# Kernel optimization log

Measured on AMD Instinct MI355X. Metric: run time of the kernel, lower is better.

## Reference

```python
import jax, jax.numpy as jnp
import numpy as np

WORD_EMB = 300   # config.word_emb_size
SEN_EMB  = 256   # config.sen_emb_size (bidirectional -> 512)
DOC_EMB  = 256   # config.doc_emb_size (bidirectional -> 512)
SEN2, DOC2 = 2 * SEN_EMB, 2 * DOC_EMB
B, S, L, TL = 64, 10, 30, 15
VOCAB, NO_URLS = 50000, 64


def setup_inputs() -> dict:
    key = jax.random.key(0)
    ks = jax.random.split(key, 32)
    def nrm(k, shape, s=0.05):
        return jax.random.normal(k, shape, jnp.float32) * s
    inp = {}
    inp["input_ids"] = jax.random.randint(ks[0], (B, S, L), 0, VOCAB)
    inp["urls"]      = jax.random.randint(ks[1], (B, S), 0, NO_URLS)
    inp["titles"]    = jax.random.randint(ks[2], (B, TL), 0, VOCAB)
    inp["emb"] = nrm(ks[3], (VOCAB, WORD_EMB), 0.1)
    # sentence BiLSTM (PyTorch gate order i,f,g,o; b = b_ih + b_hh fused)
    inp["sen_wih_f"] = nrm(ks[4], (4 * SEN_EMB, WORD_EMB))
    inp["sen_whh_f"] = nrm(ks[5], (4 * SEN_EMB, SEN_EMB))
    inp["sen_b_f"]   = nrm(ks[6], (4 * SEN_EMB,))
    inp["sen_wih_b"] = nrm(ks[7], (4 * SEN_EMB, WORD_EMB))
    inp["sen_whh_b"] = nrm(ks[8], (4 * SEN_EMB, SEN_EMB))
    inp["sen_b_b"]   = nrm(ks[9], (4 * SEN_EMB,))
    # SourceBias per-url expert weights
    inp["trans"]   = nrm(ks[10], (NO_URLS, SEN2, SEN2))
    inp["sb_bias"] = nrm(ks[11], (NO_URLS, SEN2))
    # document BiLSTM
    inp["doc_wih_f"] = nrm(ks[12], (4 * DOC_EMB, SEN2))
    inp["doc_whh_f"] = nrm(ks[13], (4 * DOC_EMB, DOC_EMB))
    inp["doc_b_f"]   = nrm(ks[14], (4 * DOC_EMB,))
    inp["doc_wih_b"] = nrm(ks[15], (4 * DOC_EMB, SEN2))
    inp["doc_whh_b"] = nrm(ks[16], (4 * DOC_EMB, DOC_EMB))
    inp["doc_b_b"]   = nrm(ks[17], (4 * DOC_EMB,))
    # Bilinear attention: out = x W y + b, W:[DOC2, SEN2]
    inp["attn_W"] = nrm(ks[18], (DOC2, SEN2))
    inp["attn_b"] = nrm(ks[19], (1,))
    # bias MLP 512 -> 256 -> 5
    inp["bias_W1"] = nrm(ks[20], (DOC2 // 2, DOC2))
    inp["bias_b1"] = nrm(ks[21], (DOC2 // 2,))
    inp["bias_W2"] = nrm(ks[22], (5, DOC2 // 2))
    inp["bias_b2"] = nrm(ks[23], (5,))
    # truth MLP 512 -> 256 -> 1
    inp["truth_W1"] = nrm(ks[24], (DOC2 // 2, DOC2))
    inp["truth_b1"] = nrm(ks[25], (DOC2 // 2,))
    inp["truth_W2"] = nrm(ks[26], (1, DOC2 // 2))
    inp["truth_b2"] = nrm(ks[27], (1,))
    return inp


def _lstm_dir(x, w_ih, w_hh, b):
    # x: [N, T, E] -> (outputs [N, T, H], final hidden [N, H])
    N = x.shape[0]
    H = w_hh.shape[1]
    xw = jnp.einsum('nte,ge->ntg', x, w_ih) + b  # precompute input projection
    def step(carry, xw_t):
        h, c = carry
        gates = xw_t + h @ w_hh.T
        i, f, g, o = jnp.split(gates, 4, axis=-1)
        c = jax.nn.sigmoid(f) * c + jax.nn.sigmoid(i) * jnp.tanh(g)
        h = jax.nn.sigmoid(o) * jnp.tanh(c)
        return (h, c), h
    h0 = jnp.zeros((N, H), x.dtype)
    (hT, _), hs = jax.lax.scan(step, (h0, h0), jnp.swapaxes(xw, 0, 1))
    return jnp.swapaxes(hs, 0, 1), hT


def _bilstm(x, wf, hf, bf, wb, hb, bb):
    out_f, hT_f = _lstm_dir(x, wf, hf, bf)
    out_b, hT_b = _lstm_dir(x[:, ::-1], wb, hb, bb)
    out = jnp.concatenate([out_f, out_b[:, ::-1]], axis=-1)
    hT = jnp.concatenate([hT_f, hT_b], axis=-1)
    return out, hT


def reference(input_ids, urls, titles, emb,
              sen_wih_f, sen_whh_f, sen_b_f, sen_wih_b, sen_whh_b, sen_b_b,
              trans, sb_bias,
              doc_wih_f, doc_whh_f, doc_b_f, doc_wih_b, doc_whh_b, doc_b_b,
              attn_W, attn_b,
              bias_W1, bias_b1, bias_W2, bias_b2,
              truth_W1, truth_b1, truth_W2, truth_b2):
    # --- sentence encoder: [B,S,L] ids -> [B,S,SEN2] ---
    words = emb[input_ids.reshape(-1)].reshape(B * S, L, WORD_EMB)
    _, sen_h = _bilstm(words, sen_wih_f, sen_whh_f, sen_b_f,
                       sen_wih_b, sen_whh_b, sen_b_b)
    sentences = sen_h.reshape(B, S, SEN2)

    # --- SourceBias: per-token url-indexed weight matmul + bias + tanh ---
    u = urls.reshape(-1)                                  # [B*S]
    sen_flat = sentences.reshape(-1, SEN2)                # [B*S, SEN2]
    biased = jnp.tanh(
        jnp.einsum('td,tde->te', sen_flat, trans[u]) + sb_bias[u]
    ).reshape(B, S, SEN2)

    # --- document encoder over (source-biased) sentences ---
    documents, _ = _bilstm(biased, doc_wih_f, doc_whh_f, doc_b_f,
                           doc_wih_b, doc_whh_b, doc_b_b)  # [B,S,DOC2]

    # --- heading encoder: titles as a single sentence ---
    title_words = emb[titles.reshape(-1)].reshape(B, TL, WORD_EMB)
    _, headings = _bilstm(title_words, sen_wih_f, sen_whh_f, sen_b_f,
                          sen_wih_b, sen_whh_b, sen_b_b)   # [B, SEN2]

    # --- bilinear attention over sentences ---
    scores = jnp.einsum('bsd,de,be->bs', documents, attn_W, headings) + attn_b[0]
    w = jax.nn.softmax(scores, axis=1)                     # [B,S]
    doc_rep = jnp.einsum('bsd,bs->bd', documents, w)       # [B,DOC2]

    # --- heads ---
    h1 = jnp.tanh(doc_rep @ bias_W1.T + bias_b1)
    bias_out = jax.nn.softmax(jnp.tanh(h1 @ bias_W2.T + bias_b2), axis=1)
    t1 = jnp.tanh(doc_rep @ truth_W1.T + truth_b1)
    truth_out = jax.nn.sigmoid(jnp.tanh(t1 @ truth_W2.T + truth_b2))
    return bias_out, truth_out
```

## Files before the change

### kernel.cpp

```cpp
#include <hip/hip_runtime.h>
#include <cstddef>

typedef short bf16x8 __attribute__((ext_vector_type(8)));
typedef float f32x4 __attribute__((ext_vector_type(4)));

__device__ __forceinline__ float sigm(float x) {
    return __builtin_amdgcn_rcpf(1.f + __expf(-x));
}
__device__ __forceinline__ float ftanh(float x) {
    float e = __expf(2.f * x);
    return 1.f - 2.f * __builtin_amdgcn_rcpf(e + 1.f);
}

__device__ __forceinline__ unsigned short f2bf(float f) {
    union { float f; unsigned u; } v; v.f = f;
    return (unsigned short)((v.u + 0x7FFFu + ((v.u >> 16) & 1u)) >> 16);
}

#define N0 (20160 * 160)
#define N1 (2048 * 160)
#define N2 (2048 * 256)

__global__ __launch_bounds__(256) void prep_cast(
    const int* __restrict__ ids, const int* __restrict__ titles,
    const float* __restrict__ emb,
    const float* __restrict__ swf, const float* __restrict__ swb,
    const float* __restrict__ dwf, const float* __restrict__ dwb,
    unsigned* __restrict__ Abf, unsigned* __restrict__ Wsen,
    unsigned* __restrict__ Wdoc)
{
    int idx = blockIdx.x * 256 + threadIdx.x;
    if (idx < N0) {
        int row = idx / 160, kk = idx - row * 160;
        int id = (row < 19200) ? ids[row] : titles[row - 19200];
        float a = 0.f, b = 0.f;
        if (kk < 150) {
            const float* s = emb + (size_t)id * 300 + kk * 2;
            a = s[0]; b = s[1];
        }
        Abf[idx] = (unsigned)f2bf(a) | ((unsigned)f2bf(b) << 16);
    } else if (idx < N0 + N1) {
        int j = idx - N0;
        int row = j / 160, kk = j - row * 160;
        const float* base = (row < 1024) ? swf + (size_t)row * 300
                                         : swb + (size_t)(row - 1024) * 300;
        float a = 0.f, b = 0.f;
        if (kk < 150) { a = base[kk * 2]; b = base[kk * 2 + 1]; }
        Wsen[j] = (unsigned)f2bf(a) | ((unsigned)f2bf(b) << 16);
    } else if (idx < N0 + N1 + N2) {
        int j = idx - N0 - N1;
        int row = j >> 8, kk = j & 255;
        const float* base = (row < 1024) ? dwf + (size_t)row * 512
                                         : dwb + (size_t)(row - 1024) * 512;
        Wdoc[j] = (unsigned)f2bf(base[kk * 2]) | ((unsigned)f2bf(base[kk * 2 + 1]) << 16);
    }
}

__global__ __launch_bounds__(256) void prep_whh(
    const float* __restrict__ swf, const float* __restrict__ swb,
    const float* __restrict__ dwf, const float* __restrict__ dwb,
    unsigned* __restrict__ WS, unsigned* __restrict__ WD)
{
    int idx = blockIdx.x * 256 + threadIdx.x;
    const float* src; unsigned* dst;
    if (idx < 262144) {
        int j = idx; int dir = j >> 17; int rem = j & 131071;
        src = (dir ? swb : swf) + ((size_t)(rem >> 7) * 256 + (rem & 127) * 2);
        dst = WS + j;
    } else {
        int j = idx - 262144; int dir = j >> 17; int rem = j & 131071;
        src = (dir ? dwb : dwf) + ((size_t)(rem >> 7) * 256 + (rem & 127) * 2);
        dst = WD + j;
    }
    *dst = (unsigned)f2bf(src[0]) | ((unsigned)f2bf(src[1]) << 16);
}

__global__ __launch_bounds__(256) void proj_mfma(
    const unsigned short* __restrict__ Abf, int M, int Kp,
    const unsigned short* __restrict__ Wbf,
    const float* __restrict__ bf_, const float* __restrict__ bb_,
    float* __restrict__ out)
{
    __shared__ unsigned short As[128 * 40];
    __shared__ unsigned short Ws[128 * 40];
    const int tid  = threadIdx.x;
    const int lane = tid & 63;
    const int w    = tid >> 6;
    const int n    = lane & 15;
    const int quad = lane >> 4;
    const int bm   = blockIdx.x * 128;
    const int by   = blockIdx.y;
    const int half = by >> 3;
    const int ug32 = (by & 7) * 32;
    const unsigned short* Wb = Wbf + (size_t)half * 1024 * Kp;
    const float* biasp = half ? bb_ : bf_;

    f32x4 acc[2][8];
#pragma unroll
    for (int rt = 0; rt < 2; rt++)
#pragma unroll
        for (int ct = 0; ct < 8; ct++) acc[rt][ct] = (f32x4){0.f, 0.f, 0.f, 0.f};

    const int chunks = Kp >> 5;
    for (int kc = 0; kc < chunks; kc++) {
        const int k0 = kc * 32;
#pragma unroll
        for (int j = 0; j < 2; j++) {
            int idx = j * 256 + tid;
            int arow = idx >> 2, qq = idx & 3;
            int grow = bm + arow; if (grow >= M) grow = M - 1;
            *(uint4*)&As[arow * 40 + qq * 8] =
                *(const uint4*)(Abf + (size_t)grow * Kp + k0 + qq * 8);
            int cc = idx >> 2;
            int wrow = (cc >> 5) * 256 + ug32 + (cc & 31);
            *(uint4*)&Ws[cc * 40 + qq * 8] =
                *(const uint4*)(Wb + (size_t)wrow * Kp + k0 + qq * 8);
        }
        __syncthreads();
        bf16x8 Aq[2], Bq[8];
#pragma unroll
        for (int rt = 0; rt < 2; rt++)
            Aq[rt] = *(const bf16x8*)&As[((w * 2 + rt) * 16 + n) * 40 + quad * 8];
#pragma unroll
        for (int ct = 0; ct < 8; ct++)
            Bq[ct] = *(const bf16x8*)&Ws[(ct * 16 + n) * 40 + quad * 8];
#pragma unroll
        for (int rt = 0; rt < 2; rt++)
#pragma unroll
            for (int ct = 0; ct < 8; ct++)
                acc[rt][ct] = __builtin_amdgcn_mfma_f32_16x16x32_bf16(
                    Aq[rt], Bq[ct], acc[rt][ct], 0, 0, 0);
        __syncthreads();
    }

#pragma unroll
    for (int s = 0; s < 2; s++) {
        const int uL = s * 16 + n;
        float b0 = biasp[ug32 + uL];
        float b1 = biasp[256 + ug32 + uL];
        float b2 = biasp[512 + ug32 + uL];
        float b3 = biasp[768 + ug32 + uL];
#pragma unroll
        for (int rt = 0; rt < 2; rt++) {
#pragma unroll
            for (int r = 0; r < 4; r++) {
                int row = bm + (w * 2 + rt) * 16 + quad * 4 + r;
                if (row >= M) continue;
                float4 o;
                o.x = acc[rt][0 + s][r] + b0;
                o.y = acc[rt][2 + s][r] + b1;
                o.z = acc[rt][4 + s][r] + b2;
                o.w = acc[rt][6 + s][r] + b3;
                *(float4*)(out + (size_t)row * 2048 + half * 1024 + (ug32 + uL) * 4) = o;
            }
        }
    }
}

__device__ __forceinline__ void pair_sync(unsigned* cnt, unsigned target) {
    __syncthreads();
    if (threadIdx.x == 0) {
        __hip_atomic_fetch_add(cnt, 1u, __ATOMIC_RELAXED, __HIP_MEMORY_SCOPE_AGENT);
        while (__hip_atomic_load(cnt, __ATOMIC_RELAXED, __HIP_MEMORY_SCOPE_AGENT) < target)
            __builtin_amdgcn_s_sleep(1);
    }
    __syncthreads();
}

__device__ __forceinline__ const float* sen_xbase(
    const float* xw, const float* xw_head, int grow_e, int t)
{
    if (grow_e < 640)       return xw + ((size_t)grow_e * 30 + t) * 2048;
    else if (grow_e < 1280) return xw + ((size_t)(grow_e - 640) * 30 + 29 - t) * 2048 + 1024;
    else if (grow_e < 1344) return xw_head + ((size_t)(grow_e - 1280) * 15 + t) * 2048;
    else                    return xw_head + ((size_t)(grow_e - 1344) * 15 + 14 - t) * 2048 + 1024;
}

__global__ __launch_bounds__(512, 2) void lstm_sen2b(
    const float* __restrict__ xw, const float* __restrict__ xw_head,
    const unsigned short* __restrict__ WhhBf,
    unsigned short* hbA, unsigned short* hbB,
    float* __restrict__ sentences, float* __restrict__ headings,
    unsigned* bars)
{
    const int tid  = threadIdx.x;
    const int lane = tid & 63;
    const int w    = tid >> 6;
    const int n    = lane & 15;
    const int quad = lane >> 4;
    const int phys = blockIdx.x;
    const int g    = (phys & 7) + (phys >> 4) * 8;
    const int p    = (phys >> 3) & 1;
    const int r0   = g * 16;
    const bool bwd  = (r0 >= 640 && r0 < 1280) || (r0 >= 1344);
    const bool head = (r0 >= 1280);
    const int tEnd = head ? 15 : 30;
    unsigned* cnt = bars + g * 16;
    const unsigned short* Wd = WhhBf + (bwd ? (size_t)262144 : 0);

    __shared__ unsigned short Hs[2][16][264];
    __shared__ float G[16][516];

    bf16x8 Bf[4][8];
#pragma unroll
    for (int ct = 0; ct < 4; ct++) {
        const int c    = ct * 16 + n;
        const int unit = p * 128 + w * 16 + (c >> 2);
        const int wrow = (c & 3) * 256 + unit;
        const unsigned short* wr = Wd + (size_t)wrow * 256;
#pragma unroll
        for (int ks = 0; ks < 8; ks++)
            Bf[ct][ks] = *(const bf16x8*)(wr + ks * 32 + quad * 8);
    }

    for (int i = tid; i < 16 * 264; i += 512) ((unsigned short*)Hs[0])[i] = 0;

    const int rE  = tid & 15;
    const int iE  = tid >> 4;
    const int ug4 = p * 128 + iE * 4;
    const int grow_e = r0 + rE;
    float cr[4] = {0.f, 0.f, 0.f, 0.f};

    const float* xptr = sen_xbase(xw, xw_head, grow_e, 0) + (size_t)ug4 * 4;
    const long long xstep = bwd ? -2048 : 2048;
    float4 xv[4];
    { const float4* xp = (const float4*)xptr;
      xv[0] = xp[0]; xv[1] = xp[1]; xv[2] = xp[2]; xv[3] = xp[3]; }

    float* fdst;
    if (!head) fdst = sentences + (size_t)(bwd ? grow_e - 640 : grow_e) * 512
                      + (bwd ? 256 : 0) + ug4;
    else       fdst = headings + (size_t)(grow_e - (bwd ? 1344 : 1280)) * 512
                      + (bwd ? 256 : 0) + ug4;

    __syncthreads();

    for (int t = 0; t < tEnd; t++) {
        const int cur = t & 1;
        unsigned short* hq = (t & 1) ? hbA : hbB;

        {
            bf16x8 Af[8];
#pragma unroll
            for (int ks = 0; ks < 8; ks++)
                Af[ks] = *(const bf16x8*)&Hs[cur][n][ks * 32 + quad * 8];
            f32x4 acc[4];
#pragma unroll
            for (int ct = 0; ct < 4; ct++) acc[ct] = (f32x4){0.f, 0.f, 0.f, 0.f};
#pragma unroll
            for (int ks = 0; ks < 8; ks++)
#pragma unroll
                for (int ct = 0; ct < 4; ct++)
                    acc[ct] = __builtin_amdgcn_mfma_f32_16x16x32_bf16(
                        Af[ks], Bf[ct][ks], acc[ct], 0, 0, 0);
#pragma unroll
            for (int ct = 0; ct < 4; ct++)
#pragma unroll
                for (int r = 0; r < 4; r++)
                    G[quad * 4 + r][w * 64 + ct * 16 + n] = acc[ct][r];
        }
        __syncthreads();

        {
            const float4* Gp = (const float4*)&G[rE][iE * 16];
            unsigned long long hpack = 0ull;
            float hout[4];
#pragma unroll
            for (int q2 = 0; q2 < 4; q2++) {
                float4 gv = Gp[q2];
                float gi = gv.x + xv[q2].x;
                float gf = gv.y + xv[q2].y;
                float gg = gv.z + xv[q2].z;
                float go = gv.w + xv[q2].w;
                float cn = sigm(gf) * cr[q2] + sigm(gi) * ftanh(gg);
                float hn = sigm(go) * ftanh(cn);
                cr[q2] = cn; hout[q2] = hn;
                hpack |= ((unsigned long long)f2bf(hn)) << (16 * q2);
            }
            const int nxt = cur ^ 1;
            *(unsigned long long*)&Hs[nxt][rE][ug4] = hpack;
            __hip_atomic_store((unsigned long long*)(hq + (size_t)grow_e * 256 + ug4),
                               hpack, __ATOMIC_RELAXED, __HIP_MEMORY_SCOPE_AGENT);
            if (t == tEnd - 1) *(float4*)fdst = *(float4*)hout;
        }

        if (t + 1 < tEnd) {
            xptr += xstep;
            const float4* xp = (const float4*)xptr;
            xv[0] = xp[0]; xv[1] = xp[1]; xv[2] = xp[2]; xv[3] = xp[3];
            pair_sync(cnt, 2u * (unsigned)(t + 1));
            {
                const int nxt   = cur ^ 1;
                const int row   = tid >> 5;
                const int chunk = tid & 31;
                const int pp    = p ^ 1;
                unsigned long long v = __hip_atomic_load(
                    (const unsigned long long*)(hq + (size_t)(r0 + row) * 256
                                                + pp * 128 + chunk * 4),
                    __ATOMIC_RELAXED, __HIP_MEMORY_SCOPE_AGENT);
                *(unsigned long long*)&Hs[nxt][row][pp * 128 + chunk * 4] = v;
            }
            __syncthreads();
        }
    }
}

__global__ __launch_bounds__(512, 2) void lstm_doc2b(
    const float* __restrict__ xw,
    const unsigned short* __restrict__ WhhBf,
    unsigned short* hdA, unsigned short* hdB,
    float* __restrict__ documents,
    unsigned* bars)
{
    const int tid  = threadIdx.x;
    const int lane = tid & 63;
    const int w    = tid >> 6;
    const int n    = lane & 15;
    const int quad = lane >> 4;
    const int phys = blockIdx.x;
    const int g    = phys & 7;
    const int p    = (phys >> 3) & 1;
    const int r0   = g * 16;
    const bool bwd = (r0 >= 64);
    unsigned* cnt = bars + g * 16;
    const unsigned short* Wd = WhhBf + (bwd ? (size_t)262144 : 0);

    __shared__ unsigned short Hs[2][16][264];
    __shared__ float G[16][516];

    bf16x8 Bf[4][8];
#pragma unroll
    for (int ct = 0; ct < 4; ct++) {
        const int c    = ct * 16 + n;
        const int unit = p * 128 + w * 16 + (c >> 2);
        const int wrow = (c & 3) * 256 + unit;
        const unsigned short* wr = Wd + (size_t)wrow * 256;
#pragma unroll
        for (int ks = 0; ks < 8; ks++)
            Bf[ct][ks] = *(const bf16x8*)(wr + ks * 32 + quad * 8);
    }

    for (int i = tid; i < 16 * 264; i += 512) ((unsigned short*)Hs[0])[i] = 0;

    const int rE  = tid & 15;
    const int iE  = tid >> 4;
    const int ug4 = p * 128 + iE * 4;
    const int grow_e = r0 + rE;
    const int seq = bwd ? grow_e - 64 : grow_e;
    float cr[4] = {0.f, 0.f, 0.f, 0.f};

    const float* xptr = (!bwd ? xw + (size_t)seq * 10 * 2048
                              : xw + ((size_t)seq * 10 + 9) * 2048 + 1024)
                        + (size_t)ug4 * 4;
    const long long xstep = bwd ? -2048 : 2048;
    float4 xv[4];
    { const float4* xp = (const float4*)xptr;
      xv[0] = xp[0]; xv[1] = xp[1]; xv[2] = xp[2]; xv[3] = xp[3]; }

    float* dptr = documents + (size_t)(seq * 10 + (bwd ? 9 : 0)) * 512
                  + (bwd ? 256 : 0) + ug4;
    const long long dstep = bwd ? -512 : 512;

    __syncthreads();

    for (int t = 0; t < 10; t++) {
        const int cur = t & 1;
        unsigned short* hq = (t & 1) ? hdA : hdB;

        {
            bf16x8 Af[8];
#pragma unroll
            for (int ks = 0; ks < 8; ks++)
                Af[ks] = *(const bf16x8*)&Hs[cur][n][ks * 32 + quad * 8];
            f32x4 acc[4];
#pragma unroll
            for (int ct = 0; ct < 4; ct++) acc[ct] = (f32x4){0.f, 0.f, 0.f, 0.f};
#pragma unroll
            for (int ks = 0; ks < 8; ks++)
#pragma unroll
                for (int ct = 0; ct < 4; ct++)
                    acc[ct] = __builtin_amdgcn_mfma_f32_16x16x32_bf16(
                        Af[ks], Bf[ct][ks], acc[ct], 0, 0, 0);
#pragma unroll
            for (int ct = 0; ct < 4; ct++)
#pragma unroll
                for (int r = 0; r < 4; r++)
                    G[quad * 4 + r][w * 64 + ct * 16 + n] = acc[ct][r];
        }
        __syncthreads();

        {
            const float4* Gp = (const float4*)&G[rE][iE * 16];
            unsigned long long hpack = 0ull;
            float hout[4];
#pragma unroll
            for (int q2 = 0; q2 < 4; q2++) {
                float4 gv = Gp[q2];
                float gi = gv.x + xv[q2].x;
                float gf = gv.y + xv[q2].y;
                float gg = gv.z + xv[q2].z;
                float go = gv.w + xv[q2].w;
                float cn = sigm(gf) * cr[q2] + sigm(gi) * ftanh(gg);
                float hn = sigm(go) * ftanh(cn);
                cr[q2] = cn; hout[q2] = hn;
                hpack |= ((unsigned long long)f2bf(hn)) << (16 * q2);
            }
            const int nxt = cur ^ 1;
            *(unsigned long long*)&Hs[nxt][rE][ug4] = hpack;
            __hip_atomic_store((unsigned long long*)(hq + (size_t)grow_e * 256 + ug4),
                               hpack, __ATOMIC_RELAXED, __HIP_MEMORY_SCOPE_AGENT);
            *(float4*)dptr = *(float4*)hout;
        }

        if (t < 9) {
            xptr += xstep;  dptr += dstep;
            const float4* xp = (const float4*)xptr;
            xv[0] = xp[0]; xv[1] = xp[1]; xv[2] = xp[2]; xv[3] = xp[3];
            pair_sync(cnt, 2u * (unsigned)(t + 1));
            {
                const int nxt   = cur ^ 1;
                const int row   = tid >> 5;
                const int chunk = tid & 31;
                const int pp    = p ^ 1;
                unsigned long long v = __hip_atomic_load(
                    (const unsigned long long*)(hq + (size_t)(r0 + row) * 256
                                                + pp * 128 + chunk * 4),
                    __ATOMIC_RELAXED, __HIP_MEMORY_SCOPE_AGENT);
                *(unsigned long long*)&Hs[nxt][row][pp * 128 + chunk * 4] = v;
            }
            __syncthreads();
        }
    }
}

__global__ __launch_bounds__(256) void source_bias(
    const float* __restrict__ sentences, const int* __restrict__ urls,
    const float* __restrict__ trans, const float* __restrict__ sb_bias,
    unsigned* __restrict__ biasedBf)
{
    const int tkn = blockIdx.x;
    const int u = urls[tkn];
    const float2* Tm = (const float2*)(trans + (size_t)u * 512 * 512);
    __shared__ float sv[512];
    for (int i = threadIdx.x; i < 512; i += 256) sv[i] = sentences[(size_t)tkn * 512 + i];
    __syncthreads();
    const int e = threadIdx.x;
    float ax = 0.f, ay = 0.f;
#pragma unroll 4
    for (int d = 0; d < 512; d++) {
        float s = sv[d];
        float2 tv = Tm[(size_t)d * 256 + e];
        ax += s * tv.x; ay += s * tv.y;
    }
    const float2 bv = ((const float2*)(sb_bias + (size_t)u * 512))[e];
    float x = ftanh(ax + bv.x), y = ftanh(ay + bv.y);
    biasedBf[(size_t)tkn * 256 + e] = (unsigned)f2bf(x) | ((unsigned)f2bf(y) << 16);
}

__global__ __launch_bounds__(256) void attn_v(
    const float* __restrict__ W, const float* __restrict__ headings,
    float* __restrict__ v)
{
    const int b = blockIdx.x;
    __shared__ float hh[512];
    for (int i = threadIdx.x; i < 512; i += 256) hh[i] = headings[(size_t)b * 512 + i];
    __syncthreads();
    for (int d = threadIdx.x; d < 512; d += 256) {
        float a = 0.f;
        const float* wr = W + (size_t)d * 512;
        for (int e = 0; e < 512; e++) a += wr[e] * hh[e];
        v[(size_t)b * 512 + d] = a;
    }
}

__global__ __launch_bounds__(256) void attn_heads(
    const float* __restrict__ documents, const float* __restrict__ v,
    const float* __restrict__ attn_b,
    const float* __restrict__ bW1, const float* __restrict__ bb1,
    const float* __restrict__ bW2, const float* __restrict__ bb2,
    const float* __restrict__ tW1, const float* __restrict__ tb1,
    const float* __restrict__ tW2, const float* __restrict__ tb2,
    float* __restrict__ out)
{
    const int b = blockIdx.x, tid = threadIdx.x;
    const int lane = tid & 63, wv_ = tid >> 6;
    __shared__ float vv[512], dr[512], h1s[256], t1s[256], sw[12], lg[5];
    for (int i = tid; i < 512; i += 256) vv[i] = v[(size_t)b * 512 + i];
    __syncthreads();
    for (int q = 0; q < 3; q++) {
        int s = q * 4 + wv_;
        float p = 0.f;
        if (s < 10) {
            const float* dp = documents + (size_t)(b * 10 + s) * 512;
            for (int d = lane; d < 512; d += 64) p += dp[d] * vv[d];
        }
#pragma unroll
        for (int off = 32; off > 0; off >>= 1) p += __shfl_down(p, off, 64);
        if (s < 10 && lane == 0) sw[s] = p + attn_b[0];
    }
    __syncthreads();
    if (tid == 0) {
        float mx = sw[0];
        for (int s = 1; s < 10; s++) mx = fmaxf(mx, sw[s]);
        float sum = 0.f;
        for (int s = 0; s < 10; s++) { sw[s] = __expf(sw[s] - mx); sum += sw[s]; }
        for (int s = 0; s < 10; s++) sw[s] /= sum;
    }
    __syncthreads();
    for (int d = tid; d < 512; d += 256) {
        float a = 0.f;
#pragma unroll
        for (int s = 0; s < 10; s++) a += sw[s] * documents[(size_t)(b * 10 + s) * 512 + d];
        dr[d] = a;
    }
    __syncthreads();
    {
        float a = bb1[tid], a2 = tb1[tid];
        const float* w1 = bW1 + (size_t)tid * 512;
        const float* w2 = tW1 + (size_t)tid * 512;
        for (int k = 0; k < 512; k++) { float x = dr[k]; a += x * w1[k]; a2 += x * w2[k]; }
        h1s[tid] = ftanh(a); t1s[tid] = ftanh(a2);
    }
    __syncthreads();
    if (tid < 5) {
        float a = bb2[tid];
        const float* wp = bW2 + (size_t)tid * 256;
        for (int k = 0; k < 256; k++) a += h1s[k] * wp[k];
        lg[tid] = ftanh(a);
    }
    if (tid == 32) {
        float a = tb2[0];
        for (int k = 0; k < 256; k++) a += t1s[k] * tW2[k];
        out[320 + b] = sigm(ftanh(a));
    }
    __syncthreads();
    if (tid == 0) {
        float mx = lg[0];
        for (int j = 1; j < 5; j++) mx = fmaxf(mx, lg[j]);
        float sum = 0.f, e[5];
        for (int j = 0; j < 5; j++) { e[j] = __expf(lg[j] - mx); sum += e[j]; }
        for (int j = 0; j < 5; j++) out[b * 5 + j] = e[j] / sum;
    }
}

extern "C" void kernel_launch(void* const* d_in, const int* in_sizes, int n_in,
                              void* d_out, int out_size, void* d_ws, size_t ws_size,
                              hipStream_t stream)
{
    (void)in_sizes; (void)n_in; (void)out_size; (void)ws_size;
    const int*   input_ids = (const int*)d_in[0];
    const int*   urls      = (const int*)d_in[1];
    const int*   titles    = (const int*)d_in[2];
    const float* emb       = (const float*)d_in[3];
    const float* sen_wih_f = (const float*)d_in[4];
    const float* sen_whh_f = (const float*)d_in[5];
    const float* sen_b_f   = (const float*)d_in[6];
    const float* sen_wih_b = (const float*)d_in[7];
    const float* sen_whh_b = (const float*)d_in[8];
    const float* sen_b_b   = (const float*)d_in[9];
    const float* trans     = (const float*)d_in[10];
    const float* sb_bias   = (const float*)d_in[11];
    const float* doc_wih_f = (const float*)d_in[12];
    const float* doc_whh_f = (const float*)d_in[13];
    const float* doc_b_f   = (const float*)d_in[14];
    const float* doc_wih_b = (const float*)d_in[15];
    const float* doc_whh_b = (const float*)d_in[16];
    const float* doc_b_b   = (const float*)d_in[17];
    const float* attn_W    = (const float*)d_in[18];
    const float* attn_b    = (const float*)d_in[19];
    const float* bias_W1   = (const float*)d_in[20];
    const float* bias_b1   = (const float*)d_in[21];
    const float* bias_W2   = (const float*)d_in[22];
    const float* bias_b2   = (const float*)d_in[23];
    const float* truth_W1  = (const float*)d_in[24];
    const float* truth_b1  = (const float*)d_in[25];
    const float* truth_W2  = (const float*)d_in[26];
    const float* truth_b2  = (const float*)d_in[27];
    float* out = (float*)d_out;

    float* ws = (float*)d_ws;
    float* xw_all      = ws;
    float* xw_head     = xw_all + (size_t)19200 * 2048;
    unsigned* biasedBf = (unsigned*)(ws + 0);
    float* xw_doc      = ws + 163840;
    float* documents   = ws + 1474560;
    float* vbuf        = ws + 1802240;

    float* slotB       = ws + 41287680;
    unsigned* Abf      = (unsigned*)slotB;
    float* sentences   = slotB;
    float* headings    = slotB + 327680;
    unsigned* WhhSbf   = (unsigned*)(slotB + 360448);
    unsigned* WhhDbf   = (unsigned*)(slotB + 622592);
    unsigned short* hbA = (unsigned short*)(slotB + 884736);
    unsigned short* hbB = (unsigned short*)(slotB + 1064960);
    unsigned short* hdA = (unsigned short*)(slotB + 1245184);
    unsigned short* hdB = (unsigned short*)(slotB + 1261568);
    unsigned* barsS    = (unsigned*)(slotB + 1277952);
    unsigned* barsD    = barsS + 88 * 16;

    unsigned* Wsen     = (unsigned*)(ws + 44513280);
    unsigned* Wdoc     = (unsigned*)(ws + 44840960);

    dim3 blk(256);

    prep_cast<<<dim3((N0 + N1 + N2 + 255) / 256), blk, 0, stream>>>(
        input_ids, titles, emb, sen_wih_f, sen_wih_b, doc_wih_f, doc_wih_b,
        Abf, Wsen, Wdoc);

    proj_mfma<<<dim3(158, 16), blk, 0, stream>>>(
        (const unsigned short*)Abf, 20160, 320,
        (const unsigned short*)Wsen, sen_b_f, sen_b_b, xw_all);

    hipMemsetAsync(barsS, 0, (88 + 8) * 16 * sizeof(unsigned), stream);
    prep_whh<<<dim3(2048), blk, 0, stream>>>(
        sen_whh_f, sen_whh_b, doc_whh_f, doc_whh_b, WhhSbf, WhhDbf);

    lstm_sen2b<<<dim3(176), dim3(512), 0, stream>>>(
        xw_all, xw_head, (const unsigned short*)WhhSbf, hbA, hbB,
        sentences, headings, barsS);

    source_bias<<<dim3(640), blk, 0, stream>>>(sentences, urls, trans, sb_bias, biasedBf);

    proj_mfma<<<dim3(5, 16), blk, 0, stream>>>(
        (const unsigned short*)biasedBf, 640, 512,
        (const unsigned short*)Wdoc, doc_b_f, doc_b_b, xw_doc);

    lstm_doc2b<<<dim3(16), dim3(512), 0, stream>>>(
        xw_doc, (const unsigned short*)WhhDbf, hdA, hdB, documents, barsD);

    attn_v<<<dim3(64), blk, 0, stream>>>(attn_W, headings, vbuf);
    attn_heads<<<dim3(64), blk, 0, stream>>>(documents, vbuf, attn_b,
                                             bias_W1, bias_b1, bias_W2, bias_b2,
                                             truth_W1, truth_b1, truth_W2, truth_b2,
                                             out);
}
```

Baseline: 563.0 us.

## Group source-bias tokens by URL to reuse expert matrices; fuse attn_v into heads

The source-bias kernel used to read a full 512x512 expert matrix once per token. It now launches one block per (url, column slice), collects the tokens that share that url, and streams each matrix element once for up to 16 tokens at a time. The aim is to cut global memory traffic on the trans tensor by roughly the number of tokens per url. Separately, the attention vector kernel is folded into attn_heads, removing one launch and the intermediate buffer. The cost is a serial matvec inside each heads block and extra LDS use and registers in the grouped kernel.

```diff
diff --git a/kernel.cpp b/kernel.cpp
--- a/kernel.cpp
+++ b/kernel.cpp
@@ -433,48 +433,77 @@
     }
 }
 
-__global__ __launch_bounds__(256) void source_bias(
+__global__ __launch_bounds__(256) void source_bias_g(
     const float* __restrict__ sentences, const int* __restrict__ urls,
     const float* __restrict__ trans, const float* __restrict__ sb_bias,
     unsigned* __restrict__ biasedBf)
 {
-    const int tkn = blockIdx.x;
-    const int u = urls[tkn];
-    const float2* Tm = (const float2*)(trans + (size_t)u * 512 * 512);
-    __shared__ float sv[512];
-    for (int i = threadIdx.x; i < 512; i += 256) sv[i] = sentences[(size_t)tkn * 512 + i];
-    __syncthreads();
-    const int e = threadIdx.x;
-    float ax = 0.f, ay = 0.f;
-#pragma unroll 4
-    for (int d = 0; d < 512; d++) {
-        float s = sv[d];
-        float2 tv = Tm[(size_t)d * 256 + e];
-        ax += s * tv.x; ay += s * tv.y;
-    }
-    const float2 bv = ((const float2*)(sb_bias + (size_t)u * 512))[e];
-    float x = ftanh(ax + bv.x), y = ftanh(ay + bv.y);
-    biasedBf[(size_t)tkn * 256 + e] = (unsigned)f2bf(x) | ((unsigned)f2bf(y) << 16);
-}
-
-__global__ __launch_bounds__(256) void attn_v(
-    const float* __restrict__ W, const float* __restrict__ headings,
-    float* __restrict__ v)
-{
-    const int b = blockIdx.x;
-    __shared__ float hh[512];
-    for (int i = threadIdx.x; i < 512; i += 256) hh[i] = headings[(size_t)b * 512 + i];
-    __syncthreads();
-    for (int d = threadIdx.x; d < 512; d += 256) {
-        float a = 0.f;
-        const float* wr = W + (size_t)d * 512;
-        for (int e = 0; e < 512; e++) a += wr[e] * hh[e];
-        v[(size_t)b * 512 + d] = a;
+    const int u   = blockIdx.x;
+    const int s   = blockIdx.y;
+    const int tid = threadIdx.x;
+    __shared__ int   toks[640];
+    __shared__ int   cntS;
+    __shared__ float sv[16][516];
+    __shared__ float red[4][64][17];
+
+    if (tid == 0) cntS = 0;
+    __syncthreads();
+    for (int i = tid; i < 640; i += 256) {
+        if (urls[i] == u) {
+            int slot = atomicAdd(&cntS, 1);
+            toks[slot] = i;
+        }
+    }
+    __syncthreads();
+    const int cnt = cntS;
+    const int dq  = tid >> 6;
+    const int eL  = tid & 63;
+    const int e   = s * 64 + eL;
+    const float* Tm = trans + (size_t)u * 512 * 512;
+
+    for (int t0 = 0; t0 < cnt; t0 += 16) {
+        const int nt = (cnt - t0 < 16) ? (cnt - t0) : 16;
+        for (int i = tid; i < 16 * 128; i += 256) {
+            int r = i >> 7, c4 = i & 127;
+            float4 v4;
+            if (r < nt) v4 = *(const float4*)(sentences + (size_t)toks[t0 + r] * 512 + c4 * 4);
+            else        v4 = (float4){0.f, 0.f, 0.f, 0.f};
+            *(float4*)&sv[r][c4 * 4] = v4;
+        }
+        __syncthreads();
+
+        float ax[16];
+#pragma unroll
+        for (int r = 0; r < 16; r++) ax[r] = 0.f;
+        for (int it = 0; it < 128; it++) {
+            const int d = it * 4 + dq;
+            float wv = Tm[(size_t)d * 512 + e];
+#pragma unroll
+            for (int r = 0; r < 16; r++) ax[r] += sv[r][d] * wv;
+        }
+#pragma unroll
+        for (int r = 0; r < 16; r++) red[dq][eL][r] = ax[r];
+        __syncthreads();
+
+        for (int o = tid; o < nt * 32; o += 256) {
+            int t  = o >> 5, ep = o & 31;
+            int c0 = ep * 2, c1 = c0 + 1;
+            float x0 = red[0][c0][t] + red[1][c0][t] + red[2][c0][t] + red[3][c0][t];
+            float x1 = red[0][c1][t] + red[1][c1][t] + red[2][c1][t] + red[3][c1][t];
+            int tkn = toks[t0 + t];
+            int eg  = s * 32 + ep;
+            const float2 bv = ((const float2*)(sb_bias + (size_t)u * 512))[eg];
+            float xx = ftanh(x0 + bv.x), yy = ftanh(x1 + bv.y);
+            biasedBf[(size_t)tkn * 256 + eg] =
+                (unsigned)f2bf(xx) | ((unsigned)f2bf(yy) << 16);
+        }
+        __syncthreads();
     }
 }
 
 __global__ __launch_bounds__(256) void attn_heads(
-    const float* __restrict__ documents, const float* __restrict__ v,
+    const float* __restrict__ documents, const float* __restrict__ W,
+    const float* __restrict__ headings,
     const float* __restrict__ attn_b,
     const float* __restrict__ bW1, const float* __restrict__ bb1,
     const float* __restrict__ bW2, const float* __restrict__ bb2,
@@ -484,8 +513,15 @@
 {
     const int b = blockIdx.x, tid = threadIdx.x;
     const int lane = tid & 63, wv_ = tid >> 6;
-    __shared__ float vv[512], dr[512], h1s[256], t1s[256], sw[12], lg[5];
-    for (int i = tid; i < 512; i += 256) vv[i] = v[(size_t)b * 512 + i];
+    __shared__ float hh[512], vv[512], dr[512], h1s[256], t1s[256], sw[12], lg[5];
+    for (int i = tid; i < 512; i += 256) hh[i] = headings[(size_t)b * 512 + i];
+    __syncthreads();
+    for (int d = tid; d < 512; d += 256) {
+        float a = 0.f;
+        const float* wr = W + (size_t)d * 512;
+        for (int e2 = 0; e2 < 512; e2++) a += wr[e2] * hh[e2];
+        vv[d] = a;
+    }
     __syncthreads();
     for (int q = 0; q < 3; q++) {
         int s = q * 4 + wv_;
@@ -584,7 +620,6 @@
     unsigned* biasedBf = (unsigned*)(ws + 0);
     float* xw_doc      = ws + 163840;
     float* documents   = ws + 1474560;
-    float* vbuf        = ws + 1802240;
 
     float* slotB       = ws + 41287680;
     unsigned* Abf      = (unsigned*)slotB;
@@ -620,7 +655,8 @@
         xw_all, xw_head, (const unsigned short*)WhhSbf, hbA, hbB,
         sentences, headings, barsS);
 
-    source_bias<<<dim3(640), blk, 0, stream>>>(sentences, urls, trans, sb_bias, biasedBf);
+    source_bias_g<<<dim3(64, 8), blk, 0, stream>>>(
+        sentences, urls, trans, sb_bias, biasedBf);
 
     proj_mfma<<<dim3(5, 16), blk, 0, stream>>>(
         (const unsigned short*)biasedBf, 640, 512,
@@ -629,8 +665,7 @@
     lstm_doc2b<<<dim3(16), dim3(512), 0, stream>>>(
         xw_doc, (const unsigned short*)WhhDbf, hdA, hdB, documents, barsD);
 
-    attn_v<<<dim3(64), blk, 0, stream>>>(attn_W, headings, vbuf);
-    attn_heads<<<dim3(64), blk, 0, stream>>>(documents, vbuf, attn_b,
+    attn_heads<<<dim3(64), blk, 0, stream>>>(documents, attn_W, headings, attn_b,
                                              bias_W1, bias_b1, bias_W2, bias_b2,
                                              truth_W1, truth_b1, truth_W2, truth_b2,
                                              out);
```

New measurement: 529.4 us. -6.0%, faster.
